# Kernel optimization log

Hardware: AMD Instinct MI355X
Metric: run time of the kernel (lower is better)

Reference implementation:

```python
import jax, jax.numpy as jnp
import numpy as np

B, T, D, H, C = 32, 512, 1024, 1024, 1000


def setup_inputs() -> dict:
    key = jax.random.key(0)
    ks = jax.random.split(key, 12)
    sc = 0.02
    return {
        "features": jax.random.normal(ks[0], (B, T, D), dtype=jnp.float32),
        "Wp": jax.random.normal(ks[1], (H, D), dtype=jnp.float32) * sc,
        "bp": jnp.zeros((H,), jnp.float32),
        "W_ih": jax.random.normal(ks[2], (3 * H, H), dtype=jnp.float32) * sc,
        "b_ih": jnp.zeros((3 * H,), jnp.float32),
        "W_hh": jax.random.normal(ks[3], (3 * H, H), dtype=jnp.float32) * sc,
        "b_hh": jnp.zeros((3 * H,), jnp.float32),
        "W1": jax.random.normal(ks[4], (H, H), dtype=jnp.float32) * sc,
        "b1": jnp.zeros((H,), jnp.float32),
        "W2": jax.random.normal(ks[5], (C, H), dtype=jnp.float32) * sc,
        "b2": jnp.zeros((C,), jnp.float32),
    }


def _gru_scan(gx, W_hh, b_hh):
    # gx: [B, T, 3H] precomputed input-side gate activations
    def step(h, gx_t):
        gh = h @ W_hh.T + b_hh                  # [B, 3H]
        xr, xz, xn = jnp.split(gx_t, 3, axis=-1)
        hr, hz, hn = jnpp if False else jnp.split(gh, 3, axis=-1)
        r = jax.nn.sigmoid(xr + hr)
        z = jax.nn.sigmoid(xz + hz)
        n = jnp.tanh(xn + r * hn)
        h_new = (1.0 - z) * n + z * h
        return h_new, h_new

    h0 = jnp.zeros((gx.shape[0], W_hh.shape[1]), gx.dtype)
    _, hs = jax.lax.scan(step, h0, jnp.swapaxes(gx, 0, 1))  # [T, B, H]
    return jnp.swapaxes(hs, 0, 1)                            # [B, T, H]


def reference(features, Wp, bp, W_ih, b_ih, W_hh, b_hh, W1, b1, W2, b2):
    # pooled inputs: relu(Linear(features))
    x = jax.nn.relu(jnp.einsum("btd,hd->bth", features, Wp) + bp)  # [B,T,H]
    # input-side gate GEMM batched over all timesteps (the recurrence only
    # needs the hidden-side GEMM per step) -- same math as per-step GRUCell
    gx = jnp.einsum("bth,gh->btg", x, W_ih) + b_ih                 # [B,T,3H]
    hs = _gru_scan(gx, W_hh, b_hh)                                  # [B,T,H]
    out = jax.nn.relu(jnp.einsum("bth,oh->bto", hs, W1) + b1)
    out = jnp.einsum("bth,ch->btc", out, W2) + b2                   # [B,T,C]
    return out
```

## Files before the change

### kernel.cpp

```cpp
#include <hip/hip_runtime.h>
#include <hip/hip_bf16.h>
#include <stdint.h>

#define Bb 32
#define Tt 512
#define Dd 1024
#define Hh 1024
#define Cc 1000
#define Mm (Bb*Tt)
#define SENT 0x7F7F7F7Fu

typedef float f32x4 __attribute__((ext_vector_type(4)));
typedef short bf16x8 __attribute__((ext_vector_type(8)));

#define MFMA16(a,b,c) __builtin_amdgcn_mfma_f32_16x16x32_bf16(a,b,c,0,0,0)

static __device__ __forceinline__ unsigned short f2b(float f){
  __hip_bfloat16 h = __float2bfloat16(f);
  union { __hip_bfloat16 h; unsigned short u; } cv; cv.h = h; return cv.u;
}
static __device__ __forceinline__ float b2f(unsigned short u){
  union { unsigned int i; float f; } cv; cv.i = ((unsigned int)u) << 16; return cv.f;
}

static __device__ __forceinline__ void async16(const ushort* g, ushort* l){
  __builtin_amdgcn_global_load_lds((const __attribute__((address_space(1))) unsigned int*)g,
                                   (__attribute__((address_space(3))) unsigned int*)l,
                                   16, 0, 0);
}

template<int FAST>
static __device__ __forceinline__ bf16x8 h_load(const ushort* p){
  bf16x8 r;
  if constexpr (FAST)
    asm volatile("global_load_dwordx4 %0, %1, off sc1" : "=v"(r) : "v"(p) : "memory");
  else
    asm volatile("global_load_dwordx4 %0, %1, off sc0 sc1" : "=v"(r) : "v"(p) : "memory");
  return r;
}
template<int FAST>
static __device__ __forceinline__ void h_store(ushort* p, unsigned int v){
  if constexpr (FAST)
    asm volatile("global_store_dword %0, %1, off sc1" :: "v"(p), "v"(v) : "memory");
  else
    asm volatile("global_store_dword %0, %1, off sc0 sc1" :: "v"(p), "v"(v) : "memory");
}

static __device__ __forceinline__ int load4sys(const int* p){
  int v;
  asm volatile("global_load_dword %0, %1, off sc0 sc1" : "=v"(v) : "v"(p) : "memory");
  asm volatile("s_waitcnt vmcnt(0)" ::: "memory");
  return v;
}
static __device__ __forceinline__ void store4sys(int* p, int v){
  asm volatile("global_store_dword %0, %1, off sc0 sc1" :: "v"(p), "v"(v) : "memory");
}


__global__ void cvt_bf16(const float* __restrict__ in, ushort* __restrict__ out, int n4){
  int i = blockIdx.x*256 + threadIdx.x;
  if (i < n4){
    const float4 v = ((const float4*)in)[i];
    ushort4 o;
    o.x = f2b(v.x); o.y = f2b(v.y); o.z = f2b(v.z); o.w = f2b(v.w);
    ((ushort4*)out)[i] = o;
  }
}

__global__ void pad_w2(const float* __restrict__ w2, const float* __restrict__ b2,
                       ushort* __restrict__ w2p, float* __restrict__ b2p){
  int i = blockIdx.x*256 + threadIdx.x;
  int r = i >> 10, c = i & 1023;
  w2p[i] = (r < Cc) ? f2b(w2[r*1024 + c]) : (ushort)0;
  if (i < 1024) b2p[i] = (i < Cc) ? b2[i] : 0.f;
}


template<int RELU, int OUT_BF16, int PERM_A, int PERM_C>
__global__ __launch_bounds__(256) void gemm_bt(
    const ushort* __restrict__ A, const ushort* __restrict__ Bm,
    const float* __restrict__ bias, void* __restrict__ Cp,
    int M, int N, int K, int ldc, int nout)
{
  __shared__ ushort As[128*32];
  __shared__ ushort Bs[128*32];
  const int tid  = threadIdx.x;
  const int lane = tid & 63;
  const int wave = tid >> 6;
  const int wr = wave >> 1, wc = wave & 1;
  const int r0 = lane & 15, kg = lane >> 4;
  const int m0 = blockIdx.x*128, n0 = blockIdx.y*128;

  const int lrA0 = m0 + (tid>>2);
  const int lrA1 = lrA0 + 64;
  const size_t prA0 = PERM_A ? (size_t)((lrA0 & 511)*32 + (lrA0 >> 9)) : (size_t)lrA0;
  const size_t prA1 = PERM_A ? (size_t)((lrA1 & 511)*32 + (lrA1 >> 9)) : (size_t)lrA1;
  const ushort* aG0 = A  + prA0*K + (tid&3)*8;
  const ushort* aG1 = A  + prA1*K + (tid&3)*8;
  const ushort* bG  = Bm + (size_t)(n0 + (tid>>2))*K + (tid&3)*8;
  ushort* aL = As + tid*8;
  ushort* bL = Bs + tid*8;
  const size_t rstep = (size_t)64*K;

  f32x4 acc[4][4] = {};

  for (int kt = 0; kt < K; kt += 32){
    __syncthreads();
    async16(aG0 + kt, aL);
    async16(aG1 + kt, aL + 2048);
    async16(bG + kt,         bL);
    async16(bG + kt + rstep, bL + 2048);
    __syncthreads();
    bf16x8 af[4], bf_[4];
#pragma unroll
    for (int i=0;i<4;i++) af[i]  = *(const bf16x8*)&As[(wr*64 + i*16 + r0)*32 + kg*8];
#pragma unroll
    for (int j=0;j<4;j++) bf_[j] = *(const bf16x8*)&Bs[(wc*64 + j*16 + r0)*32 + kg*8];
#pragma unroll
    for (int i=0;i<4;i++)
#pragma unroll
      for (int j=0;j<4;j++)
        acc[i][j] = MFMA16(af[i], bf_[j], acc[i][j]);
  }

  const int rowb = m0 + wr*64 + kg*4;
  const int colb = n0 + wc*64 + r0;
#pragma unroll
  for (int i=0;i<4;i++){
#pragma unroll
    for (int j=0;j<4;j++){
      const int c = colb + j*16;
      if (c >= nout) continue;
      const float bv = bias ? bias[c] : 0.f;
#pragma unroll
      for (int q=0;q<4;q++){
        const int r = rowb + i*16 + q;
        const size_t pr = PERM_C ? (size_t)((r & 511)*32 + (r >> 9)) : (size_t)r;
        float v = acc[i][j][q] + bv;
        if (RELU) v = fmaxf(v, 0.f);
        if (OUT_BF16) ((ushort*)Cp)[pr*ldc + c] = f2b(v);
        else          ((float* )Cp)[pr*ldc + c] = v;
      }
    }
  }
}


#define REDN 4656

template<int FAST>
static __device__ __forceinline__ void scan_body(
    const int g, const int m, const int tid,
    const ushort* __restrict__ Whh, const float* __restrict__ bhh,
    const ushort* __restrict__ gxT, ushort* __restrict__ hsAll,
    float* __restrict__ red)
{
  const int wave = tid >> 6;
  const int lane = tid & 63;
  const int r0 = lane & 15, kg = lane >> 4;
  const int kbase = wave*128 + kg*8;

  bf16x8 wb[6][4];
#pragma unroll
  for (int n=0;n<6;n++){
    const ushort* wr_ = Whh + ((size_t)((n>>1)*1024 + m*32 + (n&1)*16 + r0))*1024 + kbase;
#pragma unroll
    for (int ks=0;ks<4;ks++)
      wb[n][ks] = *(const bf16x8*)(wr_ + ks*32);
  }

  const int eb = tid >> 4;
  const int u0 = (tid & 15)*2;
  const int jg = m*32 + u0;
  float br0=0,br1=0,bz0=0,bz1=0,bn0=0,bn1=0;
  if (tid < 64){
    br0 = bhh[jg];       br1 = bhh[jg+1];
    bz0 = bhh[1024+jg];  bz1 = bhh[1024+jg+1];
    bn0 = bhh[2048+jg];  bn1 = bhh[2048+jg+1];
  }
  float hold0 = 0.f, hold1 = 0.f;

  unsigned xr=0, xz=0, xn=0, xrN=0, xzN=0, xnN=0;
  if (tid < 64){
    const ushort* gb = gxT + (size_t)(g*4 + eb)*3072 + jg;
    asm volatile("global_load_dword %0, %1, off" : "=v"(xr) : "v"(gb));
    asm volatile("global_load_dword %0, %1, off" : "=v"(xz) : "v"(gb + 1024));
    asm volatile("global_load_dword %0, %1, off" : "=v"(xn) : "v"(gb + 2048));
  }

  for (int t = 0; t < Tt; ++t){
    const int buf = t & 1;

    const ushort* aB = hsAll + (size_t)(t*32 + g*4 + (r0 & 3))*1024 + kbase;
    bf16x8 ha[4];
    int again;
    do {
#pragma unroll
      for (int ks=0;ks<4;ks++) ha[ks] = h_load<FAST>(aB + ks*32);
      asm volatile("s_waitcnt vmcnt(0)" ::: "memory");
      __builtin_amdgcn_sched_barrier(0);
      unsigned sent = 0;
#pragma unroll
      for (int ks=0;ks<4;ks++){
        union { bf16x8 v; unsigned u[4]; } A; A.v = ha[ks];
#pragma unroll
        for (int q=0;q<4;q++) sent |= (A.u[q] == SENT);
      }
      again = __any((int)sent);
    } while (again);

    if (tid < 64 && t+1 < Tt){
      const ushort* gb = gxT + (size_t)((t+1)*32 + g*4 + eb)*3072 + jg;
      asm volatile("global_load_dword %0, %1, off" : "=v"(xrN) : "v"(gb));
      asm volatile("global_load_dword %0, %1, off" : "=v"(xzN) : "v"(gb + 1024));
      asm volatile("global_load_dword %0, %1, off" : "=v"(xnN) : "v"(gb + 2048));
    }

    f32x4 acc[6] = {};
#pragma unroll
    for (int ks=0;ks<4;ks++)
#pragma unroll
      for (int n=0;n<6;n++)
        acc[n] = MFMA16(ha[ks], wb[n][ks], acc[n]);

    if (kg == 0){
      float* rb = red + buf*REDN;
#pragma unroll
      for (int n=0;n<6;n++)
#pragma unroll
        for (int q=0;q<4;q++)
          rb[(q*97 + n*16 + r0)*12 + wave] = acc[n][q];
    }
    __syncthreads();

    if (tid < 64){
      const float* rb = red + buf*REDN;
      float s[6];
#pragma unroll
      for (int i=0;i<6;i++){
        const int g3 = i >> 1, du = i & 1;
        const int slot = eb*97 + g3*32 + u0 + du;
        const float4 a  = *(const float4*)&rb[slot*12];
        const float4 b4 = *(const float4*)&rb[slot*12 + 4];
        s[i] = (a.x + a.y) + (a.z + a.w) + (b4.x + b4.y) + (b4.z + b4.w);
      }
      float h0, h1;
      {
        const float r = 1.f/(1.f + __expf(-(b2f((ushort)(xr & 0xffff)) + s[0] + br0)));
        const float z = 1.f/(1.f + __expf(-(b2f((ushort)(xz & 0xffff)) + s[2] + bz0)));
        const float a = b2f((ushort)(xn & 0xffff)) + r*(s[4] + bn0);
        const float e = __expf(-2.f*a);
        const float n = (1.f - e)/(1.f + e);
        h0 = (1.f - z)*n + z*hold0; hold0 = h0;
      }
      {
        const float r = 1.f/(1.f + __expf(-(b2f((ushort)(xr >> 16)) + s[1] + br1)));
        const float z = 1.f/(1.f + __expf(-(b2f((ushort)(xz >> 16)) + s[3] + bz1)));
        const float a = b2f((ushort)(xn >> 16)) + r*(s[5] + bn1);
        const float e = __expf(-2.f*a);
        const float n = (1.f - e)/(1.f + e);
        h1 = (1.f - z)*n + z*hold1; hold1 = h1;
      }
      const unsigned packed = (unsigned)f2b(h0) | ((unsigned)f2b(h1) << 16);
      h_store<FAST>(hsAll + (size_t)((t+1)*32 + g*4 + eb)*1024 + jg, packed);
      xr = xrN; xz = xzN; xn = xnN;
    }
  }
}

__global__ __launch_bounds__(512, 1) void gru_scan(
    const ushort* __restrict__ Whh, const float* __restrict__ bhh,
    const ushort* __restrict__ gxT,
    ushort* __restrict__ hsAll,
    int* __restrict__ xccTab)
{
  __shared__ float red[2*REDN];
  __shared__ int fastFlag;
  const int bid = blockIdx.x;
  const int g = bid & 7, m = bid >> 3;
  const int tid = threadIdx.x;
  int* decTab = xccTab + 256;

  if (tid == 0){
    int myxcc;
    asm volatile("s_getreg_b32 %0, hwreg(HW_REG_XCC_ID)" : "=s"(myxcc));
    store4sys(&xccTab[bid], myxcc);
    if (m == 0){
      int ok = 1;
      long budget = 200000;
      for (int p = 0; p < 32 && ok; ++p){
        int v;
        do {
          v = load4sys(&xccTab[p*8 + g]);
          if (v == -1){ __builtin_amdgcn_s_sleep(1); if (--budget <= 0){ ok = 0; break; } }
        } while (v == -1);
        if (v != myxcc) ok = 0;
      }
      store4sys(&decTab[g], ok);
      fastFlag = ok;
    } else {
      int v;
      do {
        v = load4sys(&decTab[g]);
        if (v == -1) __builtin_amdgcn_s_sleep(1);
      } while (v == -1);
      fastFlag = v;
    }
  }
  __syncthreads();

  if (fastFlag) scan_body<1>(g, m, tid, Whh, bhh, gxT, hsAll, red);
  else          scan_body<0>(g, m, tid, Whh, bhh, gxT, hsAll, red);
}


extern "C" void kernel_launch(void* const* d_in, const int* in_sizes, int n_in,
                              void* d_out, int out_size, void* d_ws, size_t ws_size,
                              hipStream_t stream)
{
  const float* features = (const float*)d_in[0];
  const float* Wp  = (const float*)d_in[1];
  const float* bp  = (const float*)d_in[2];
  const float* Wih = (const float*)d_in[3];
  const float* bih = (const float*)d_in[4];
  const float* Whh = (const float*)d_in[5];
  const float* bhh = (const float*)d_in[6];
  const float* W1  = (const float*)d_in[7];
  const float* b1  = (const float*)d_in[8];
  const float* W2  = (const float*)d_in[9];
  const float* b2  = (const float*)d_in[10];
  float* out = (float*)d_out;

  char* w = (char*)d_ws;
  auto alloc = [&](size_t bytes){ char* p = w; w += (bytes + 255) & ~(size_t)255; return p; };
  ushort* fb    = (ushort*)alloc((size_t)Mm*Dd*2);
  ushort* xb    = (ushort*)alloc((size_t)Mm*Hh*2);
  ushort* gxT   = (ushort*)alloc((size_t)Mm*3*Hh*2);
  ushort* hsAll = (ushort*)alloc((size_t)(Tt+1)*Bb*Hh*2);
  ushort* o1    = (ushort*)alloc((size_t)Mm*Hh*2);
  ushort* wpb   = (ushort*)alloc((size_t)Hh*Dd*2);
  ushort* wihb  = (ushort*)alloc((size_t)3*Hh*Hh*2);
  ushort* whhb  = (ushort*)alloc((size_t)3*Hh*Hh*2);
  ushort* w1b   = (ushort*)alloc((size_t)Hh*Hh*2);
  ushort* w2b   = (ushort*)alloc((size_t)1024*Hh*2);
  float*  b2p   = (float*)alloc(1024*4);
  int*    xccTab= (int*)alloc(264*4);
  ushort* hsT   = hsAll + (size_t)Bb*Hh;

  hipMemsetAsync(hsAll, 0x7F, (size_t)(Tt+1)*Bb*Hh*2, stream);
  hipMemsetAsync(hsAll, 0x00, (size_t)Bb*Hh*2, stream);
  hipMemsetAsync(xccTab, 0xFF, 264*4, stream);

  auto cvt = [&](const float* src, ushort* dst, size_t n){
    int n4 = (int)(n/4);
    hipLaunchKernelGGL(cvt_bf16, dim3((n4+255)/256), dim3(256), 0, stream, src, dst, n4);
  };
  cvt(features, fb, (size_t)Mm*Dd);
  cvt(Wp,  wpb,  (size_t)Hh*Dd);
  cvt(Wih, wihb, (size_t)3*Hh*Hh);
  cvt(Whh, whhb, (size_t)3*Hh*Hh);
  cvt(W1,  w1b,  (size_t)Hh*Hh);
  hipLaunchKernelGGL(pad_w2, dim3((1024*1024)/256), dim3(256), 0, stream, W2, b2, w2b, b2p);

  hipLaunchKernelGGL((gemm_bt<1,1,0,0>), dim3(Mm/128, Hh/128), dim3(256), 0, stream,
                     fb, wpb, bp, (void*)xb, Mm, Hh, Dd, Hh, Hh);
  hipLaunchKernelGGL((gemm_bt<0,1,0,1>), dim3(Mm/128, (3*Hh)/128), dim3(256), 0, stream,
                     xb, wihb, bih, (void*)gxT, Mm, 3*Hh, Hh, 3*Hh, 3*Hh);

  hipLaunchKernelGGL(gru_scan, dim3(256), dim3(512), 0, stream,
                     whhb, bhh, gxT, hsAll, xccTab);

  hipLaunchKernelGGL((gemm_bt<1,1,1,0>), dim3(Mm/128, Hh/128), dim3(256), 0, stream,
                     hsT, w1b, b1, (void*)o1, Mm, Hh, Hh, Hh, Hh);
  hipLaunchKernelGGL((gemm_bt<0,0,0,0>), dim3(Mm/128, 1024/128), dim3(256), 0, stream,
                     o1, w2b, b2p, (void*)out, Mm, 1024, Hh, Cc, Cc);
}
```

Measured before the change: 1.924 ms.

## Fuse W1 projection into GRU scan and add XCD-aware GEMM block swizzle

Each scan block now keeps a 32-row slice of W1 in registers. Every step it multiplies the previously polled hidden state by that slice, reduces the result through a second LDS buffer, applies bias and ReLU, and writes o1 in time-major order. This removes the separate W1 GEMM launch and its re-read of all hidden states. The final GEMM reads o1 with permuted rows, and the scan loop runs two extra iterations to drain the lagged output. GEMM block indices are also remapped so neighbouring tiles land on the same XCD. The risk is that the extra MFMAs, LDS traffic and reduction work sit inside the latency-bound recurrence step.

```diff
diff --git a/kernel.cpp b/kernel.cpp
--- a/kernel.cpp
+++ b/kernel.cpp
@@ -89,7 +89,14 @@
   const int wave = tid >> 6;
   const int wr = wave >> 1, wc = wave & 1;
   const int r0 = lane & 15, kg = lane >> 4;
-  const int m0 = blockIdx.x*128, n0 = blockIdx.y*128;
+
+  const int nwg = gridDim.x * gridDim.y;
+  const int lin = blockIdx.y * gridDim.x + blockIdx.x;
+  const int cpx = nwg >> 3;
+  const int swz = (lin & 7) * cpx + (lin >> 3);
+  const int bx = swz % gridDim.x, by = swz / gridDim.x;
+
+  const int m0 = bx*128, n0 = by*128;
 
   const int lrA0 = m0 + (tid>>2);
   const int lrA1 = lrA0 + 64;
@@ -146,14 +153,16 @@
 }
 
 
-#define REDN 4656
+#define REDN  4656
+#define REDN2 1584
 
 template<int FAST>
 static __device__ __forceinline__ void scan_body(
     const int g, const int m, const int tid,
     const ushort* __restrict__ Whh, const float* __restrict__ bhh,
+    const ushort* __restrict__ W1b, const float* __restrict__ b1,
     const ushort* __restrict__ gxT, ushort* __restrict__ hsAll,
-    float* __restrict__ red)
+    ushort* __restrict__ o1, float* __restrict__ red, float* __restrict__ red2)
 {
   const int wave = tid >> 6;
   const int lane = tid & 63;
@@ -167,6 +176,14 @@
 #pragma unroll
     for (int ks=0;ks<4;ks++)
       wb[n][ks] = *(const bf16x8*)(wr_ + ks*32);
+  }
+  bf16x8 w1f[2][4];
+#pragma unroll
+  for (int n2=0;n2<2;n2++){
+    const ushort* wr_ = W1b + ((size_t)(m*32 + n2*16 + r0))*1024 + kbase;
+#pragma unroll
+    for (int ks=0;ks<4;ks++)
+      w1f[n2][ks] = *(const bf16x8*)(wr_ + ks*32);
   }
 
   const int eb = tid >> 4;
@@ -178,6 +195,13 @@
     bz0 = bhh[1024+jg];  bz1 = bhh[1024+jg+1];
     bn0 = bhh[2048+jg];  bn1 = bhh[2048+jg+1];
   }
+  const int t2  = tid & 63;
+  const int eb2 = t2 >> 4;
+  const int u02 = (t2 & 15)*2;
+  const int jg2 = m*32 + u02;
+  float b1a=0, b1b=0;
+  if (tid >= 64 && tid < 128){ b1a = b1[jg2]; b1b = b1[jg2+1]; }
+
   float hold0 = 0.f, hold1 = 0.f;
 
   unsigned xr=0, xz=0, xn=0, xrN=0, xzN=0, xnN=0;
@@ -188,26 +212,53 @@
     asm volatile("global_load_dword %0, %1, off" : "=v"(xn) : "v"(gb + 2048));
   }
 
-  for (int t = 0; t < Tt; ++t){
+  bf16x8 ha[4], haP[4];
+
+  for (int t = 0; t <= Tt+1; ++t){
     const int buf = t & 1;
+    const int polled = (t <= Tt);
 
     const ushort* aB = hsAll + (size_t)(t*32 + g*4 + (r0 & 3))*1024 + kbase;
-    bf16x8 ha[4];
-    int again;
-    do {
+    if (polled){
 #pragma unroll
       for (int ks=0;ks<4;ks++) ha[ks] = h_load<FAST>(aB + ks*32);
-      asm volatile("s_waitcnt vmcnt(0)" ::: "memory");
-      __builtin_amdgcn_sched_barrier(0);
-      unsigned sent = 0;
-#pragma unroll
-      for (int ks=0;ks<4;ks++){
-        union { bf16x8 v; unsigned u[4]; } A; A.v = ha[ks];
-#pragma unroll
-        for (int q=0;q<4;q++) sent |= (A.u[q] == SENT);
-      }
-      again = __any((int)sent);
-    } while (again);
+    }
+
+    if (t >= 2){
+      f32x4 acc2[2] = {};
+#pragma unroll
+      for (int ks=0;ks<4;ks++)
+#pragma unroll
+        for (int n2=0;n2<2;n2++)
+          acc2[n2] = MFMA16(haP[ks], w1f[n2][ks], acc2[n2]);
+      if (kg == 0){
+        float* rb2 = red2 + buf*REDN2;
+#pragma unroll
+        for (int n2=0;n2<2;n2++)
+#pragma unroll
+          for (int q=0;q<4;q++)
+            rb2[(q*33 + n2*16 + r0)*12 + wave] = acc2[n2][q];
+      }
+    }
+
+    if (polled){
+      int again;
+      for(;;){
+        asm volatile("s_waitcnt vmcnt(0)" ::: "memory");
+        __builtin_amdgcn_sched_barrier(0);
+        unsigned sent = 0;
+#pragma unroll
+        for (int ks=0;ks<4;ks++){
+          union { bf16x8 v; unsigned u[4]; } A; A.v = ha[ks];
+#pragma unroll
+          for (int q=0;q<4;q++) sent |= (A.u[q] == SENT);
+        }
+        again = __any((int)sent);
+        if (!again) break;
+#pragma unroll
+        for (int ks=0;ks<4;ks++) ha[ks] = h_load<FAST>(aB + ks*32);
+      }
+    }
 
     if (tid < 64 && t+1 < Tt){
       const ushort* gb = gxT + (size_t)((t+1)*32 + g*4 + eb)*3072 + jg;
@@ -216,24 +267,26 @@
       asm volatile("global_load_dword %0, %1, off" : "=v"(xnN) : "v"(gb + 2048));
     }
 
-    f32x4 acc[6] = {};
-#pragma unroll
-    for (int ks=0;ks<4;ks++)
-#pragma unroll
-      for (int n=0;n<6;n++)
-        acc[n] = MFMA16(ha[ks], wb[n][ks], acc[n]);
-
-    if (kg == 0){
-      float* rb = red + buf*REDN;
-#pragma unroll
-      for (int n=0;n<6;n++)
-#pragma unroll
-        for (int q=0;q<4;q++)
-          rb[(q*97 + n*16 + r0)*12 + wave] = acc[n][q];
-    }
+    if (t < Tt){
+      f32x4 acc[6] = {};
+#pragma unroll
+      for (int ks=0;ks<4;ks++)
+#pragma unroll
+        for (int n=0;n<6;n++)
+          acc[n] = MFMA16(ha[ks], wb[n][ks], acc[n]);
+      if (kg == 0){
+        float* rb = red + buf*REDN;
+#pragma unroll
+        for (int n=0;n<6;n++)
+#pragma unroll
+          for (int q=0;q<4;q++)
+            rb[(q*97 + n*16 + r0)*12 + wave] = acc[n][q];
+      }
+    }
+
     __syncthreads();
 
-    if (tid < 64){
+    if (t < Tt && tid < 64){
       const float* rb = red + buf*REDN;
       float s[6];
 #pragma unroll
@@ -265,16 +318,45 @@
       h_store<FAST>(hsAll + (size_t)((t+1)*32 + g*4 + eb)*1024 + jg, packed);
       xr = xrN; xz = xzN; xn = xnN;
     }
+
+    if (t >= 2 && tid >= 64 && tid < 128){
+      const float* rb2 = red2 + buf*REDN2;
+      float s0, s1;
+      {
+        const int slot = eb2*33 + u02;
+        const float4 a  = *(const float4*)&rb2[slot*12];
+        const float4 b4 = *(const float4*)&rb2[slot*12 + 4];
+        s0 = (a.x + a.y) + (a.z + a.w) + (b4.x + b4.y) + (b4.z + b4.w);
+      }
+      {
+        const int slot = eb2*33 + u02 + 1;
+        const float4 a  = *(const float4*)&rb2[slot*12];
+        const float4 b4 = *(const float4*)&rb2[slot*12 + 4];
+        s1 = (a.x + a.y) + (a.z + a.w) + (b4.x + b4.y) + (b4.z + b4.w);
+      }
+      const float o0 = fmaxf(s0 + b1a, 0.f);
+      const float o1v = fmaxf(s1 + b1b, 0.f);
+      const unsigned packed = (unsigned)f2b(o0) | ((unsigned)f2b(o1v) << 16);
+      *(unsigned*)(o1 + (size_t)((t-2)*32 + g*4 + eb2)*1024 + jg2) = packed;
+    }
+
+    if (polled){
+#pragma unroll
+      for (int ks=0;ks<4;ks++) haP[ks] = ha[ks];
+    }
   }
 }
 
 __global__ __launch_bounds__(512, 1) void gru_scan(
     const ushort* __restrict__ Whh, const float* __restrict__ bhh,
+    const ushort* __restrict__ W1b, const float* __restrict__ b1,
     const ushort* __restrict__ gxT,
     ushort* __restrict__ hsAll,
+    ushort* __restrict__ o1,
     int* __restrict__ xccTab)
 {
   __shared__ float red[2*REDN];
+  __shared__ float red2[2*REDN2];
   __shared__ int fastFlag;
   const int bid = blockIdx.x;
   const int g = bid & 7, m = bid >> 3;
@@ -309,8 +391,8 @@
   }
   __syncthreads();
 
-  if (fastFlag) scan_body<1>(g, m, tid, Whh, bhh, gxT, hsAll, red);
-  else          scan_body<0>(g, m, tid, Whh, bhh, gxT, hsAll, red);
+  if (fastFlag) scan_body<1>(g, m, tid, Whh, bhh, W1b, b1, gxT, hsAll, o1, red, red2);
+  else          scan_body<0>(g, m, tid, Whh, bhh, W1b, b1, gxT, hsAll, o1, red, red2);
 }
 
 
@@ -345,7 +427,6 @@
   ushort* w2b   = (ushort*)alloc((size_t)1024*Hh*2);
   float*  b2p   = (float*)alloc(1024*4);
   int*    xccTab= (int*)alloc(264*4);
-  ushort* hsT   = hsAll + (size_t)Bb*Hh;
 
   hipMemsetAsync(hsAll, 0x7F, (size_t)(Tt+1)*Bb*Hh*2, stream);
   hipMemsetAsync(hsAll, 0x00, (size_t)Bb*Hh*2, stream);
@@ -368,10 +449,8 @@
                      xb, wihb, bih, (void*)gxT, Mm, 3*Hh, Hh, 3*Hh, 3*Hh);
 
   hipLaunchKernelGGL(gru_scan, dim3(256), dim3(512), 0, stream,
-                     whhb, bhh, gxT, hsAll, xccTab);
-
-  hipLaunchKernelGGL((gemm_bt<1,1,1,0>), dim3(Mm/128, Hh/128), dim3(256), 0, stream,
-                     hsT, w1b, b1, (void*)o1, Mm, Hh, Hh, Hh, Hh);
-  hipLaunchKernelGGL((gemm_bt<0,0,0,0>), dim3(Mm/128, 1024/128), dim3(256), 0, stream,
+                     whhb, bhh, w1b, b1, gxT, hsAll, o1, xccTab);
+
+  hipLaunchKernelGGL((gemm_bt<0,0,1,0>), dim3(Mm/128, 1024/128), dim3(256), 0, stream,
                      o1, w2b, b2p, (void*)out, Mm, 1024, Hh, Cc, Cc);
 }
```

Measured after the change: 1.882 ms. 1.02x faster.
